# Optimization experiments

Measured on AMD Instinct MI355X. Metric: run time of the kernel, lower is better.

Reference implementation:

```python
import jax, jax.numpy as jnp
import numpy as np
import math

THETA = 10000.0

def _rope(x, pos):
    # x: [B, H, S, Dh], pos: [S]
    d = x.shape[-1]
    inv_freq = 1.0 / (THETA ** (jnp.arange(0, d, 2, dtype=jnp.float32) / d))  # [Dh/2]
    ang = pos.astype(jnp.float32)[:, None] * inv_freq[None, :]                # [S, Dh/2]
    cos, sin = jnp.cos(ang), jnp.sin(ang)
    x1, x2 = x[..., 0::2], x[..., 1::2]
    r1 = x1 * cos - x2 * sin
    r2 = x1 * sin + x2 * cos
    return jnp.stack([r1, r2], axis=-1).reshape(x.shape)

def setup_inputs() -> dict:
    key = jax.random.key(0)
    ks = jax.random.split(key, 5)
    B, S, D = 2, 1024, 2048
    Dkv = 512
    scale = 1.0 / math.sqrt(D)
    return {
        "X": jax.random.normal(ks[0], (B, S, D), dtype=jnp.float32),
        "token_positions": jnp.arange(S, dtype=jnp.int32),
        "q_w": jax.random.normal(ks[1], (D, D), dtype=jnp.float32) * scale,
        "k_w": jax.random.normal(ks[2], (Dkv, D), dtype=jnp.float32) * scale,
        "v_w": jax.random.normal(ks[3], (Dkv, D), dtype=jnp.float32) * scale,
        "o_w": jax.random.normal(ks[4], (D, D), dtype=jnp.float32) * scale,
    }

def reference(X, token_positions, q_w, k_w, v_w, o_w):
    B, S, D = X.shape
    H, Hkv = 32, 8
    Dh = D // H
    G = H // Hkv  # query heads per KV head

    Q = (X @ q_w.T).reshape(B, S, H, Dh).transpose(0, 2, 1, 3)      # [B,H,S,Dh]
    K = (X @ k_w.T).reshape(B, S, Hkv, Dh).transpose(0, 2, 1, 3)    # [B,Hkv,S,Dh]
    V = (X @ v_w.T).reshape(B, S, Hkv, Dh).transpose(0, 2, 1, 3)    # [B,Hkv,S,Dh]

    Q = _rope(Q, token_positions)
    K = _rope(K, token_positions)

    # group query heads: [B, Hkv, G, S, Dh]
    Qg = Q.reshape(B, Hkv, G, S, Dh)
    scores = jnp.einsum('bkgqd,bkld->bkgql', Qg, K) / math.sqrt(Dh)  # [B,Hkv,G,S,S]
    causal = jnp.tril(jnp.ones((S, S), dtype=bool))
    scores = jnp.where(causal, scores, -jnp.inf)
    probs = jax.nn.softmax(scores, axis=-1)
    attn = jnp.einsum('bkgql,bkld->bkgqd', probs, V)                 # [B,Hkv,G,S,Dh]

    attn = attn.reshape(B, H, S, Dh).transpose(0, 2, 1, 3).reshape(B, S, D)
    return attn @ o_w.T
```

## Files before the change

kernel.cpp:

```cpp
#include <hip/hip_runtime.h>

typedef _Float16 f16;
typedef _Float16 half8 __attribute__((ext_vector_type(8), may_alias));
typedef _Float16 half4 __attribute__((ext_vector_type(4), may_alias));
typedef float f32x4 __attribute__((ext_vector_type(4), may_alias));

#define ROPE_KF -0.41524101186092027f

__device__ __forceinline__ void gload_lds16(const f16* g, f16* lds) {
  __builtin_amdgcn_global_load_lds(
      (const __attribute__((address_space(1))) void*)g,
      (__attribute__((address_space(3))) void*)lds, 16, 0, 0);
}

template <int N>
__device__ __forceinline__ void waitcnt_vm() {
  if constexpr (N == 0) asm volatile("s_waitcnt vmcnt(0)" ::: "memory");
  else if constexpr (N == 3) asm volatile("s_waitcnt vmcnt(3)" ::: "memory");
  else if constexpr (N == 4) asm volatile("s_waitcnt vmcnt(4)" ::: "memory");
}

__device__ __forceinline__ half8 rope8(half8 v, float posf, int i0, float scale) {
  half8 r;
#pragma unroll
  for (int p = 0; p < 4; ++p) {
    const float ang = posf * exp2f(ROPE_KF * (float)(i0 + p));
    float s, c;
    sincosf(ang, &s, &c);
    const float x1 = (float)v[2 * p], x2 = (float)v[2 * p + 1];
    r[2 * p]     = (f16)((x1 * c - x2 * s) * scale);
    r[2 * p + 1] = (f16)((x1 * s + x2 * c) * scale);
  }
  return r;
}

__global__ __launch_bounds__(256) void cvt_all(const float* __restrict__ s0, f16* __restrict__ d0, int n0,
                                               const float* __restrict__ s1, f16* __restrict__ d1, int n1,
                                               const float* __restrict__ s2, f16* __restrict__ d2, int n2,
                                               const float* __restrict__ s3, f16* __restrict__ d3, int n3,
                                               const float* __restrict__ s4, f16* __restrict__ d4, int n4) {
  const int step = gridDim.x * blockDim.x * 4;
  const int base = (blockIdx.x * blockDim.x + threadIdx.x) * 4;
  auto go = [&](const float* s, f16* d, int n) {
    for (int i = base; i < n; i += step) {
      float4 v = *(const float4*)(s + i);
      half4 h;
      h[0] = (f16)v.x; h[1] = (f16)v.y; h[2] = (f16)v.z; h[3] = (f16)v.w;
      *(half4*)(d + i) = h;
    }
  };
  go(s0, d0, n0); go(s1, d1, n1); go(s2, d2, n2); go(s3, d3, n3); go(s4, d4, n4);
}

template <int OUT_F32, int BM>
__global__ __launch_bounds__(256, 2) void gemm_bt(const f16* __restrict__ A,
                                                  const f16* __restrict__ B,
                                                  void* __restrict__ Cv,
                                                  int M, int N, int K) {
  constexpr int NJ = (BM == 128) ? 4 : 2;
  constexpr int ACH = BM / 64;
  constexpr int LPS = ACH + 2;

  __shared__ alignas(16) f16 As[2][BM][32];
  __shared__ alignas(16) f16 Bs[2][128][32];
  const int tid = threadIdx.x;
  const int w = tid >> 6, l = tid & 63;
  const int m0 = blockIdx.y * BM, n0 = blockIdx.x << 7;
  const int fr = l & 15;
  const int fkz = (((l >> 4) ^ ((fr >> 1) & 3)) << 3);
  const int wr = (BM == 128) ? ((w >> 1) << 6) : 0;
  const int wc = (BM == 128) ? ((w & 1) << 6) : (w << 5);
  const int srow = l >> 2;
  const int scol = (((l & 3) ^ ((l >> 3) & 3)) << 3);

  const f16* ga = A + (size_t)(m0 + srow) * K + scol;
  const f16* gb = B + (size_t)(n0 + srow) * K + scol;

  auto stage = [&](int buf, int t) {
    const int k0 = t << 5;
#pragma unroll
    for (int c = 0; c < ACH; ++c) {
      const int rb = (w * ACH + c) << 4;
      gload_lds16(ga + (size_t)rb * K + k0, &As[buf][rb][0]);
    }
#pragma unroll
    for (int c = 0; c < 2; ++c) {
      const int rb = (w * 2 + c) << 4;
      gload_lds16(gb + (size_t)rb * K + k0, &Bs[buf][rb][0]);
    }
  };

  f32x4 acc[4][NJ] = {};

  const int nk = K >> 5;
  stage(0, 0);
  stage(1, 1);
  for (int t = 0; t < nk; ++t) {
    const int buf = t & 1;
    if (t + 1 < nk) waitcnt_vm<LPS>();
    else waitcnt_vm<0>();
    __builtin_amdgcn_s_barrier();
    __builtin_amdgcn_sched_barrier(0);
    half8 af[4], bf[NJ];
#pragma unroll
    for (int i = 0; i < 4; ++i) af[i] = *(const half8*)&As[buf][wr + i * 16 + fr][fkz];
#pragma unroll
    for (int j = 0; j < NJ; ++j) bf[j] = *(const half8*)&Bs[buf][wc + j * 16 + fr][fkz];
#pragma unroll
    for (int i = 0; i < 4; ++i)
#pragma unroll
      for (int j = 0; j < NJ; ++j)
        acc[i][j] = __builtin_amdgcn_mfma_f32_16x16x32_f16(af[i], bf[j], acc[i][j], 0, 0, 0);
    __builtin_amdgcn_sched_barrier(0);
    __builtin_amdgcn_s_barrier();
    if (t + 2 < nk) stage(buf, t + 2);
  }

  const int orow = (l >> 4) << 2;
#pragma unroll
  for (int i = 0; i < 4; ++i) {
#pragma unroll
    for (int j = 0; j < NJ; ++j) {
      const int col = n0 + wc + j * 16 + fr;
#pragma unroll
      for (int r = 0; r < 4; ++r) {
        const size_t idx = (size_t)(m0 + wr + i * 16 + orow + r) * N + col;
        if (OUT_F32) ((float*)Cv)[idx] = acc[i][j][r];
        else ((f16*)Cv)[idx] = (f16)acc[i][j][r];
      }
    }
  }
}

__global__ __launch_bounds__(256) void repack_kv(const f16* __restrict__ QKV,
                                                 const int* __restrict__ pos,
                                                 f16* __restrict__ Kp,
                                                 f16* __restrict__ Vt) {
  const int kt = blockIdx.x, kvh = blockIdx.y, b = blockIdx.z;
  const int tid = threadIdx.x;
  __shared__ f16 vs[64][72];
  const size_t tile = ((size_t)((b * 8 + kvh) * 16 + kt)) * 4096;
  const f16* kbase = QKV + 2048 + kvh * 64;
  const f16* vbase = QKV + 2560 + kvh * 64;
#pragma unroll
  for (int p = 0; p < 2; ++p) {
    const int c = tid + p * 256;
    const int row = c >> 3, slot = c & 7;
    const size_t grow = (size_t)(b * 1024 + kt * 64 + row) * 3072;
    half8 kk = *(const half8*)(kbase + grow + slot * 8);
    kk = rope8(kk, (float)pos[kt * 64 + row], slot << 2, 1.0f);
    *(half8*)(Kp + tile + row * 64 + ((slot ^ (row & 7)) << 3)) = kk;
    *(half8*)&vs[row][slot * 8] = *(const half8*)(vbase + grow + slot * 8);
  }
  __syncthreads();
#pragma unroll
  for (int p = 0; p < 2; ++p) {
    const int c = tid + p * 256;
    const int d = c >> 3, oct = c & 7;
    half8 vv;
#pragma unroll
    for (int m = 0; m < 8; ++m) vv[m] = vs[oct * 8 + m][d];
    *(half8*)(Vt + tile + d * 64 + ((oct ^ (d & 7)) << 3)) = vv;
  }
}

__global__ __launch_bounds__(256) void attn_fwd(const f16* __restrict__ QKV,
                                                const f16* __restrict__ Kp,
                                                const f16* __restrict__ Vt,
                                                const int* __restrict__ pos,
                                                f16* __restrict__ O) {
  const int flat = blockIdx.x + (blockIdx.y << 3) + (blockIdx.z << 8);
  const int rmid = ((flat & 7) << 6) + (flat >> 3);
  const int pr = rmid & 7, h = (rmid >> 3) & 31, b = rmid >> 8;
  const int kvh = h >> 2;
  const int tid = threadIdx.x, w = tid >> 6, l = tid & 63;
  const int fr = l & 15, g = l >> 4;
  const int orow = g << 2;
  const int qtA = pr, qtB = 15 - pr;

  __shared__ alignas(16) char KsB[2][8192];
  __shared__ alignas(16) char VtB[2][8192];
  __shared__ alignas(16) f16 Ps[4][16][72];

  auto KS = [&](int buf, int row, int slot) -> f16* {
    return (f16*)(KsB[buf] + row * 128 + ((slot ^ (row & 7)) << 4));
  };
  auto VT = [&](int buf, int d, int oct) -> f16* {
    return (f16*)(VtB[buf] + d * 128 + ((oct ^ (d & 7)) << 4));
  };

  const int sA = qtA * 64 + w * 16 + fr, sB = qtB * 64 + w * 16 + fr;
  const float pA = (float)pos[sA], pB = (float)pos[sB];
  const size_t qoff = (size_t)(b * 1024 + w * 16 + fr) * 3072 + h * 64 + (g << 3);
  const f16* qA = QKV + qoff + (size_t)qtA * 64 * 3072;
  const f16* qB = QKV + qoff + (size_t)qtB * 64 * 3072;
  const half8 aA0 = rope8(*(const half8*)qA, pA, g << 2, 0.125f);
  const half8 aA1 = rope8(*(const half8*)(qA + 32), pA, 16 + (g << 2), 0.125f);
  const half8 aB0 = rope8(*(const half8*)qB, pB, g << 2, 0.125f);
  const half8 aB1 = rope8(*(const half8*)(qB + 32), pB, 16 + (g << 2), 0.125f);

  float rmA[4], rlA[4], rmB[4], rlB[4];
  f32x4 oA[4] = {}, oB[4] = {};
#pragma unroll
  for (int r = 0; r < 4; ++r) { rmA[r] = rmB[r] = -3.0e38f; rlA[r] = rlB[r] = 0.f; }

  const size_t tbase = ((size_t)((b * 8 + kvh) * 16)) * 4096;
  const f16* kp0 = Kp + tbase + w * 1024 + (l << 3);
  const f16* vp0 = Vt + tbase + w * 1024 + (l << 3);
  auto stage = [&](int buf, int kt) {
    const f16* kp = kp0 + (size_t)kt * 4096;
    const f16* vp = vp0 + (size_t)kt * 4096;
    f16* kl = (f16*)(KsB[buf] + w * 2048);
    f16* vl = (f16*)(VtB[buf] + w * 2048);
    gload_lds16(kp, kl);
    gload_lds16(kp + 512, kl + 512);
    gload_lds16(vp, vl);
    gload_lds16(vp + 512, vl + 512);
  };

  auto compute = [&](int buf, const half8& a0, const half8& a1, float* rm, float* rl,
                     f32x4* o, int qt, int kt) {
    f32x4 s4[4] = {};
#pragma unroll
    for (int j = 0; j < 4; ++j) {
      const half8 bk0 = *(const half8*)KS(buf, j * 16 + fr, g);
      const half8 bk1 = *(const half8*)KS(buf, j * 16 + fr, 4 + g);
      s4[j] = __builtin_amdgcn_mfma_f32_16x16x32_f16(a0, bk0, s4[j], 0, 0, 0);
      s4[j] = __builtin_amdgcn_mfma_f32_16x16x32_f16(a1, bk1, s4[j], 0, 0, 0);
    }
    if (kt == qt) {
      const int qrow0 = qt * 64 + w * 16 + orow;
#pragma unroll
      for (int j = 0; j < 4; ++j) {
        const int col = kt * 64 + j * 16 + fr;
#pragma unroll
        for (int r = 0; r < 4; ++r)
          if (col > qrow0 + r) s4[j][r] = -1.0e30f;
      }
    }
#pragma unroll
    for (int r = 0; r < 4; ++r) {
      float mx = fmaxf(fmaxf(s4[0][r], s4[1][r]), fmaxf(s4[2][r], s4[3][r]));
#pragma unroll
      for (int off = 8; off >= 1; off >>= 1) mx = fmaxf(mx, __shfl_xor(mx, off));
      const float mn = fmaxf(rm[r], mx);
      const float sf = __expf(rm[r] - mn);
      rl[r] *= sf;
      o[0][r] *= sf; o[1][r] *= sf; o[2][r] *= sf; o[3][r] *= sf;
      rm[r] = mn;
    }
    float ps[4] = {0.f, 0.f, 0.f, 0.f};
#pragma unroll
    for (int j = 0; j < 4; ++j)
#pragma unroll
      for (int r = 0; r < 4; ++r) {
        const float p = __expf(s4[j][r] - rm[r]);
        ps[r] += p;
        Ps[w][orow + r][j * 16 + fr] = (f16)p;
      }
#pragma unroll
    for (int r = 0; r < 4; ++r) {
      float t = ps[r];
#pragma unroll
      for (int off = 8; off >= 1; off >>= 1) t += __shfl_xor(t, off);
      rl[r] += t;
    }
#pragma unroll
    for (int kv2 = 0; kv2 < 2; ++kv2) {
      const half8 ap = *(const half8*)&Ps[w][fr][kv2 * 32 + (g << 3)];
#pragma unroll
      for (int j = 0; j < 4; ++j) {
        const half8 bv = *(const half8*)VT(buf, j * 16 + fr, kv2 * 4 + g);
        o[j] = __builtin_amdgcn_mfma_f32_16x16x32_f16(ap, bv, o[j], 0, 0, 0);
      }
    }
  };

  stage(0, 0);
  stage(1, 1);
  for (int kt = 0; kt <= qtB; ++kt) {
    const int buf = kt & 1;
    if (kt < qtB) waitcnt_vm<4>();
    else waitcnt_vm<0>();
    __builtin_amdgcn_s_barrier();
    __builtin_amdgcn_sched_barrier(0);
    if (kt <= qtA) compute(buf, aA0, aA1, rmA, rlA, oA, qtA, kt);
    compute(buf, aB0, aB1, rmB, rlB, oB, qtB, kt);
    __builtin_amdgcn_sched_barrier(0);
    __builtin_amdgcn_s_barrier();
    if (kt + 2 <= qtB) stage(buf, kt + 2);
  }

#pragma unroll
  for (int j = 0; j < 4; ++j)
#pragma unroll
    for (int r = 0; r < 4; ++r) {
      const int rowA = qtA * 64 + w * 16 + orow + r;
      const int rowB = qtB * 64 + w * 16 + orow + r;
      const int col = h * 64 + j * 16 + fr;
      O[(size_t)(b * 1024 + rowA) * 2048 + col] = (f16)(oA[j][r] / rlA[r]);
      O[(size_t)(b * 1024 + rowB) * 2048 + col] = (f16)(oB[j][r] / rlB[r]);
    }
}

extern "C" void kernel_launch(void* const* d_in, const int* in_sizes, int n_in,
                              void* d_out, int out_size, void* d_ws, size_t ws_size,
                              hipStream_t stream) {
  const float* X = (const float*)d_in[0];
  const int* tokpos = (const int*)d_in[1];
  const float* qw = (const float*)d_in[2];
  const float* kw = (const float*)d_in[3];
  const float* vw = (const float*)d_in[4];
  const float* ow = (const float*)d_in[5];

  constexpr int B = 2, S = 1024, D = 2048, DKV = 512, H = 32;
  constexpr int M = B * S;
  constexpr int NQKV = D + 2 * DKV;

  char* ws = (char*)d_ws;
  f16* Xh   = (f16*)(ws);
  f16* QKVW = (f16*)(ws + (8u << 20));
  f16* owh  = (f16*)(ws + (20u << 20));
  f16* QKVc = (f16*)(ws + (28u << 20));
  f16* Ah   = (f16*)(ws + (40u << 20));
  f16* Kp   = (f16*)(ws);
  f16* Vt   = (f16*)(ws + (2u << 20));

  cvt_all<<<2048, 256, 0, stream>>>(X, Xh, M * D,
                                    qw, QKVW, D * D,
                                    kw, QKVW + (size_t)D * D, DKV * D,
                                    vw, QKVW + (size_t)(D + DKV) * D, DKV * D,
                                    ow, owh, D * D);

  gemm_bt<0, 128><<<dim3(NQKV / 128, M / 128), 256, 0, stream>>>(Xh, QKVW, QKVc, M, NQKV, D);

  repack_kv<<<dim3(16, 8, 2), 256, 0, stream>>>(QKVc, tokpos, Kp, Vt);

  attn_fwd<<<dim3(8, H, B), 256, 0, stream>>>(QKVc, Kp, Vt, tokpos, Ah);

  gemm_bt<1, 64><<<dim3(D / 128, M / 64), 256, 0, stream>>>(Ah, owh, d_out, M, D, D);
}
```

Measured before the change: 137.5 us.

## Deepen GEMM pipeline to four LDS stages with register-prefetched fragments

The GEMM kernel moves from a two-stage to a four-stage LDS ring buffer and keeps three tiles in flight. It double-buffers the MFMA operand fragments in registers, so the next tile's LDS reads overlap the current tile's MFMAs. The trailing barrier per k-step is dropped, leaving one barrier per step. In exchange it uses twice the LDS and more VGPRs, which could reduce occupancy at two blocks per CU.

Measured after the change: 142.7 us. 3.8% more time.

```diff
diff --git a/kernel.cpp b/kernel.cpp
--- a/kernel.cpp
+++ b/kernel.cpp
@@ -14,10 +14,12 @@
 }
 
 template <int N>
-__device__ __forceinline__ void waitcnt_vm() {
+__device__ __forceinline__ void vm_wait() {
   if constexpr (N == 0) asm volatile("s_waitcnt vmcnt(0)" ::: "memory");
   else if constexpr (N == 3) asm volatile("s_waitcnt vmcnt(3)" ::: "memory");
   else if constexpr (N == 4) asm volatile("s_waitcnt vmcnt(4)" ::: "memory");
+  else if constexpr (N == 6) asm volatile("s_waitcnt vmcnt(6)" ::: "memory");
+  else if constexpr (N == 8) asm volatile("s_waitcnt vmcnt(8)" ::: "memory");
 }
 
 __device__ __forceinline__ half8 rope8(half8 v, float posf, int i0, float scale) {
@@ -61,8 +63,8 @@
   constexpr int ACH = BM / 64;
   constexpr int LPS = ACH + 2;
 
-  __shared__ alignas(16) f16 As[2][BM][32];
-  __shared__ alignas(16) f16 Bs[2][128][32];
+  __shared__ alignas(16) f16 As[4][BM][32];
+  __shared__ alignas(16) f16 Bs[4][128][32];
   const int tid = threadIdx.x;
   const int w = tid >> 6, l = tid & 63;
   const int m0 = blockIdx.y * BM, n0 = blockIdx.x << 7;
@@ -76,8 +78,8 @@
   const f16* ga = A + (size_t)(m0 + srow) * K + scol;
   const f16* gb = B + (size_t)(n0 + srow) * K + scol;
 
-  auto stage = [&](int buf, int t) {
-    const int k0 = t << 5;
+  auto stage = [&](int t) {
+    const int buf = t & 3, k0 = t << 5;
 #pragma unroll
     for (int c = 0; c < ACH; ++c) {
       const int rb = (w * ACH + c) << 4;
@@ -90,30 +92,48 @@
     }
   };
 
+  half8 afA[4], bfA[NJ], afB[4], bfB[NJ];
+  auto readfrags = [&](int t, half8* af, half8* bf) {
+    const int buf = t & 3;
+#pragma unroll
+    for (int i = 0; i < 4; ++i) af[i] = *(const half8*)&As[buf][wr + i * 16 + fr][fkz];
+#pragma unroll
+    for (int j = 0; j < NJ; ++j) bf[j] = *(const half8*)&Bs[buf][wc + j * 16 + fr][fkz];
+  };
+
   f32x4 acc[4][NJ] = {};
+  auto mm = [&](half8* af, half8* bf) {
+#pragma unroll
+    for (int i = 0; i < 4; ++i)
+#pragma unroll
+      for (int j = 0; j < NJ; ++j)
+        acc[i][j] = __builtin_amdgcn_mfma_f32_16x16x32_f16(af[i], bf[j], acc[i][j], 0, 0, 0);
+  };
 
   const int nk = K >> 5;
-  stage(0, 0);
-  stage(1, 1);
-  for (int t = 0; t < nk; ++t) {
-    const int buf = t & 1;
-    if (t + 1 < nk) waitcnt_vm<LPS>();
-    else waitcnt_vm<0>();
+  stage(0); stage(1); stage(2);
+  vm_wait<2 * LPS>();
+  __builtin_amdgcn_s_barrier();
+  __builtin_amdgcn_sched_barrier(0);
+  readfrags(0, afA, bfA);
+
+  for (int t = 0; t < nk; t += 2) {
+    if (t + 2 < nk) vm_wait<LPS>(); else vm_wait<0>();
     __builtin_amdgcn_s_barrier();
     __builtin_amdgcn_sched_barrier(0);
-    half8 af[4], bf[NJ];
-#pragma unroll
-    for (int i = 0; i < 4; ++i) af[i] = *(const half8*)&As[buf][wr + i * 16 + fr][fkz];
-#pragma unroll
-    for (int j = 0; j < NJ; ++j) bf[j] = *(const half8*)&Bs[buf][wc + j * 16 + fr][fkz];
-#pragma unroll
-    for (int i = 0; i < 4; ++i)
-#pragma unroll
-      for (int j = 0; j < NJ; ++j)
-        acc[i][j] = __builtin_amdgcn_mfma_f32_16x16x32_f16(af[i], bf[j], acc[i][j], 0, 0, 0);
+    if (t + 3 < nk) stage(t + 3);
+    if (t + 1 < nk) readfrags(t + 1, afB, bfB);
+    mm(afA, bfA);
     __builtin_amdgcn_sched_barrier(0);
-    __builtin_amdgcn_s_barrier();
-    if (t + 2 < nk) stage(buf, t + 2);
+    if (t + 1 < nk) {
+      if (t + 3 < nk) vm_wait<LPS>(); else vm_wait<0>();
+      __builtin_amdgcn_s_barrier();
+      __builtin_amdgcn_sched_barrier(0);
+      if (t + 4 < nk) stage(t + 4);
+      if (t + 2 < nk) readfrags(t + 2, afA, bfA);
+      mm(afB, bfB);
+      __builtin_amdgcn_sched_barrier(0);
+    }
   }
 
   const int orow = (l >> 4) << 2;
@@ -280,8 +300,8 @@
   stage(1, 1);
   for (int kt = 0; kt <= qtB; ++kt) {
     const int buf = kt & 1;
-    if (kt < qtB) waitcnt_vm<4>();
-    else waitcnt_vm<0>();
+    if (kt < qtB) vm_wait<4>();
+    else vm_wait<0>();
     __builtin_amdgcn_s_barrier();
     __builtin_amdgcn_sched_barrier(0);
     if (kt <= qtA) compute(buf, aA0, aA1, rmA, rlA, oA, qtA, kt);
```

## Rewrite GEMM as single-wave 128x64 tiles with 4-stage barrier-free pipeline

Applied to the files above, without the earlier changes.

Replaces the 256-thread, 4-wave GEMM with a 64-thread, single-wavefront kernel. Each wave computes a 128x64 output tile with an 8x4 MFMA accumulator and uses a 4-deep LDS ring buffer, prefetching two stages ahead and waiting only on vmcnt. Because one wave owns the whole tile, the workgroup barriers go away and more tiles can be resident per CU. The cost is much higher register pressure per wave (128 accumulator floats) and less parallelism per block, which may hurt latency hiding. Both the QKV and output projections now use this kernel.

After: 170.4 us. 23.9% more time.

```diff
diff --git a/kernel.cpp b/kernel.cpp
--- a/kernel.cpp
+++ b/kernel.cpp
@@ -14,10 +14,11 @@
 }
 
 template <int N>
-__device__ __forceinline__ void waitcnt_vm() {
+__device__ __forceinline__ void vm_wait() {
   if constexpr (N == 0) asm volatile("s_waitcnt vmcnt(0)" ::: "memory");
-  else if constexpr (N == 3) asm volatile("s_waitcnt vmcnt(3)" ::: "memory");
   else if constexpr (N == 4) asm volatile("s_waitcnt vmcnt(4)" ::: "memory");
+  else if constexpr (N == 12) asm volatile("s_waitcnt vmcnt(12)" ::: "memory");
+  else if constexpr (N == 24) asm volatile("s_waitcnt vmcnt(24)" ::: "memory");
 }
 
 __device__ __forceinline__ half8 rope8(half8 v, float posf, int i0, float scale) {
@@ -52,79 +53,70 @@
   go(s0, d0, n0); go(s1, d1, n1); go(s2, d2, n2); go(s3, d3, n3); go(s4, d4, n4);
 }
 
-template <int OUT_F32, int BM>
-__global__ __launch_bounds__(256, 2) void gemm_bt(const f16* __restrict__ A,
-                                                  const f16* __restrict__ B,
-                                                  void* __restrict__ Cv,
-                                                  int M, int N, int K) {
-  constexpr int NJ = (BM == 128) ? 4 : 2;
-  constexpr int ACH = BM / 64;
-  constexpr int LPS = ACH + 2;
-
-  __shared__ alignas(16) f16 As[2][BM][32];
-  __shared__ alignas(16) f16 Bs[2][128][32];
-  const int tid = threadIdx.x;
-  const int w = tid >> 6, l = tid & 63;
-  const int m0 = blockIdx.y * BM, n0 = blockIdx.x << 7;
+template <int OUT_F32>
+__global__ __launch_bounds__(64) void gemm_bt(const f16* __restrict__ A,
+                                              const f16* __restrict__ B,
+                                              void* __restrict__ Cv,
+                                              int M, int N, int K) {
+  __shared__ alignas(16) f16 As[4][128][32];
+  __shared__ alignas(16) f16 Bs[4][64][32];
+  const int l = threadIdx.x;
+  const int m0 = blockIdx.y << 7, n0 = blockIdx.x << 6;
   const int fr = l & 15;
   const int fkz = (((l >> 4) ^ ((fr >> 1) & 3)) << 3);
-  const int wr = (BM == 128) ? ((w >> 1) << 6) : 0;
-  const int wc = (BM == 128) ? ((w & 1) << 6) : (w << 5);
   const int srow = l >> 2;
   const int scol = (((l & 3) ^ ((l >> 3) & 3)) << 3);
 
   const f16* ga = A + (size_t)(m0 + srow) * K + scol;
   const f16* gb = B + (size_t)(n0 + srow) * K + scol;
 
-  auto stage = [&](int buf, int t) {
-    const int k0 = t << 5;
-#pragma unroll
-    for (int c = 0; c < ACH; ++c) {
-      const int rb = (w * ACH + c) << 4;
-      gload_lds16(ga + (size_t)rb * K + k0, &As[buf][rb][0]);
-    }
-#pragma unroll
-    for (int c = 0; c < 2; ++c) {
-      const int rb = (w * 2 + c) << 4;
-      gload_lds16(gb + (size_t)rb * K + k0, &Bs[buf][rb][0]);
-    }
-  };
-
-  f32x4 acc[4][NJ] = {};
+  auto stage = [&](int t) {
+    const int buf = t & 3, k0 = t << 5;
+#pragma unroll
+    for (int c = 0; c < 8; ++c)
+      gload_lds16(ga + (size_t)(c << 4) * K + k0, &As[buf][c << 4][0]);
+#pragma unroll
+    for (int c = 0; c < 4; ++c)
+      gload_lds16(gb + (size_t)(c << 4) * K + k0, &Bs[buf][c << 4][0]);
+  };
+
+  f32x4 acc[8][4] = {};
 
   const int nk = K >> 5;
-  stage(0, 0);
-  stage(1, 1);
+  stage(0);
+  stage(1);
   for (int t = 0; t < nk; ++t) {
-    const int buf = t & 1;
-    if (t + 1 < nk) waitcnt_vm<LPS>();
-    else waitcnt_vm<0>();
-    __builtin_amdgcn_s_barrier();
+    if (t + 2 < nk) {
+      stage(t + 2);
+      vm_wait<24>();
+    } else if (t + 1 < nk) {
+      vm_wait<12>();
+    } else {
+      vm_wait<0>();
+    }
     __builtin_amdgcn_sched_barrier(0);
-    half8 af[4], bf[NJ];
-#pragma unroll
-    for (int i = 0; i < 4; ++i) af[i] = *(const half8*)&As[buf][wr + i * 16 + fr][fkz];
-#pragma unroll
-    for (int j = 0; j < NJ; ++j) bf[j] = *(const half8*)&Bs[buf][wc + j * 16 + fr][fkz];
-#pragma unroll
-    for (int i = 0; i < 4; ++i)
-#pragma unroll
-      for (int j = 0; j < NJ; ++j)
+    const int buf = t & 3;
+    half8 af[8], bf[4];
+#pragma unroll
+    for (int j = 0; j < 4; ++j) bf[j] = *(const half8*)&Bs[buf][j * 16 + fr][fkz];
+#pragma unroll
+    for (int i = 0; i < 8; ++i) af[i] = *(const half8*)&As[buf][i * 16 + fr][fkz];
+#pragma unroll
+    for (int i = 0; i < 8; ++i)
+#pragma unroll
+      for (int j = 0; j < 4; ++j)
         acc[i][j] = __builtin_amdgcn_mfma_f32_16x16x32_f16(af[i], bf[j], acc[i][j], 0, 0, 0);
-    __builtin_amdgcn_sched_barrier(0);
-    __builtin_amdgcn_s_barrier();
-    if (t + 2 < nk) stage(buf, t + 2);
   }
 
   const int orow = (l >> 4) << 2;
 #pragma unroll
-  for (int i = 0; i < 4; ++i) {
-#pragma unroll
-    for (int j = 0; j < NJ; ++j) {
-      const int col = n0 + wc + j * 16 + fr;
+  for (int i = 0; i < 8; ++i) {
+#pragma unroll
+    for (int j = 0; j < 4; ++j) {
+      const int col = n0 + j * 16 + fr;
 #pragma unroll
       for (int r = 0; r < 4; ++r) {
-        const size_t idx = (size_t)(m0 + wr + i * 16 + orow + r) * N + col;
+        const size_t idx = (size_t)(m0 + i * 16 + orow + r) * N + col;
         if (OUT_F32) ((float*)Cv)[idx] = acc[i][j][r];
         else ((f16*)Cv)[idx] = (f16)acc[i][j][r];
       }
@@ -280,8 +272,8 @@
   stage(1, 1);
   for (int kt = 0; kt <= qtB; ++kt) {
     const int buf = kt & 1;
-    if (kt < qtB) waitcnt_vm<4>();
-    else waitcnt_vm<0>();
+    if (kt < qtB) vm_wait<4>();
+    else vm_wait<0>();
     __builtin_amdgcn_s_barrier();
     __builtin_amdgcn_sched_barrier(0);
     if (kt <= qtA) compute(buf, aA0, aA1, rmA, rlA, oA, qtA, kt);
@@ -332,11 +324,11 @@
                                     vw, QKVW + (size_t)(D + DKV) * D, DKV * D,
                                     ow, owh, D * D);
 
-  gemm_bt<0, 128><<<dim3(NQKV / 128, M / 128), 256, 0, stream>>>(Xh, QKVW, QKVc, M, NQKV, D);
+  gemm_bt<0><<<dim3(NQKV / 64, M / 128), 64, 0, stream>>>(Xh, QKVW, QKVc, M, NQKV, D);
 
   repack_kv<<<dim3(16, 8, 2), 256, 0, stream>>>(QKVc, tokpos, Kp, Vt);
 
   attn_fwd<<<dim3(8, H, B), 256, 0, stream>>>(QKVc, Kp, Vt, tokpos, Ah);
 
-  gemm_bt<1, 64><<<dim3(D / 128, M / 64), 256, 0, stream>>>(Ah, owh, d_out, M, D, D);
-}
+  gemm_bt<1><<<dim3(D / 64, M / 128), 64, 0, stream>>>(Ah, owh, d_out, M, D, D);
+}
```

## Split-K the QKV projection GEMM and fold the partial sums into consumers

Applied to the files above, without the earlier changes.

The QKV GEMM is launched with two K-splits along gridDim.z. Each split writes its own fp16 partial result buffer (QKVc0 and QKVc1), and repack_kv and attn_fwd add the two partials when they load Q, K and V. The QKV grid is only 24x16 = 384 blocks, so this doubles the parallelism to better fill the many CUs. The cost is extra partial-buffer writes and reads, and the partials are rounded to fp16 before they are summed, which loses some precision. Ah is moved in the workspace to make room for the second buffer.

Result: faster. 132.0 us (median of 5 runs) (-4.0%).

```diff
diff --git a/kernel.cpp b/kernel.cpp
--- a/kernel.cpp
+++ b/kernel.cpp
@@ -14,20 +14,22 @@
 }
 
 template <int N>
-__device__ __forceinline__ void waitcnt_vm() {
+__device__ __forceinline__ void vm_wait() {
   if constexpr (N == 0) asm volatile("s_waitcnt vmcnt(0)" ::: "memory");
   else if constexpr (N == 3) asm volatile("s_waitcnt vmcnt(3)" ::: "memory");
   else if constexpr (N == 4) asm volatile("s_waitcnt vmcnt(4)" ::: "memory");
 }
 
-__device__ __forceinline__ half8 rope8(half8 v, float posf, int i0, float scale) {
+__device__ __forceinline__ half8 rope8s(half8 va, half8 vb, float posf, int i0,
+                                        float scale) {
   half8 r;
 #pragma unroll
   for (int p = 0; p < 4; ++p) {
     const float ang = posf * exp2f(ROPE_KF * (float)(i0 + p));
     float s, c;
     sincosf(ang, &s, &c);
-    const float x1 = (float)v[2 * p], x2 = (float)v[2 * p + 1];
+    const float x1 = (float)va[2 * p] + (float)vb[2 * p];
+    const float x2 = (float)va[2 * p + 1] + (float)vb[2 * p + 1];
     r[2 * p]     = (f16)((x1 * c - x2 * s) * scale);
     r[2 * p + 1] = (f16)((x1 * s + x2 * c) * scale);
   }
@@ -66,6 +68,8 @@
   const int tid = threadIdx.x;
   const int w = tid >> 6, l = tid & 63;
   const int m0 = blockIdx.y * BM, n0 = blockIdx.x << 7;
+  const int klen = K / gridDim.z;
+  const int koff = blockIdx.z * klen;
   const int fr = l & 15;
   const int fkz = (((l >> 4) ^ ((fr >> 1) & 3)) << 3);
   const int wr = (BM == 128) ? ((w >> 1) << 6) : 0;
@@ -73,8 +77,8 @@
   const int srow = l >> 2;
   const int scol = (((l & 3) ^ ((l >> 3) & 3)) << 3);
 
-  const f16* ga = A + (size_t)(m0 + srow) * K + scol;
-  const f16* gb = B + (size_t)(n0 + srow) * K + scol;
+  const f16* ga = A + (size_t)(m0 + srow) * K + koff + scol;
+  const f16* gb = B + (size_t)(n0 + srow) * K + koff + scol;
 
   auto stage = [&](int buf, int t) {
     const int k0 = t << 5;
@@ -92,13 +96,13 @@
 
   f32x4 acc[4][NJ] = {};
 
-  const int nk = K >> 5;
   stage(0, 0);
   stage(1, 1);
+  const int nk = klen >> 5;
   for (int t = 0; t < nk; ++t) {
     const int buf = t & 1;
-    if (t + 1 < nk) waitcnt_vm<LPS>();
-    else waitcnt_vm<0>();
+    if (t + 1 < nk) vm_wait<LPS>();
+    else vm_wait<0>();
     __builtin_amdgcn_s_barrier();
     __builtin_amdgcn_sched_barrier(0);
     half8 af[4], bf[NJ];
@@ -116,6 +120,7 @@
     if (t + 2 < nk) stage(buf, t + 2);
   }
 
+  const size_t zoff = (size_t)blockIdx.z * M * (size_t)N;
   const int orow = (l >> 4) << 2;
 #pragma unroll
   for (int i = 0; i < 4; ++i) {
@@ -124,7 +129,7 @@
       const int col = n0 + wc + j * 16 + fr;
 #pragma unroll
       for (int r = 0; r < 4; ++r) {
-        const size_t idx = (size_t)(m0 + wr + i * 16 + orow + r) * N + col;
+        const size_t idx = zoff + (size_t)(m0 + wr + i * 16 + orow + r) * N + col;
         if (OUT_F32) ((float*)Cv)[idx] = acc[i][j][r];
         else ((f16*)Cv)[idx] = (f16)acc[i][j][r];
       }
@@ -132,7 +137,8 @@
   }
 }
 
-__global__ __launch_bounds__(256) void repack_kv(const f16* __restrict__ QKV,
+__global__ __launch_bounds__(256) void repack_kv(const f16* __restrict__ QKV0,
+                                                 const f16* __restrict__ QKV1,
                                                  const int* __restrict__ pos,
                                                  f16* __restrict__ Kp,
                                                  f16* __restrict__ Vt) {
@@ -140,17 +146,22 @@
   const int tid = threadIdx.x;
   __shared__ f16 vs[64][72];
   const size_t tile = ((size_t)((b * 8 + kvh) * 16 + kt)) * 4096;
-  const f16* kbase = QKV + 2048 + kvh * 64;
-  const f16* vbase = QKV + 2560 + kvh * 64;
+  const size_t kcol = 2048 + kvh * 64, vcol = 2560 + kvh * 64;
 #pragma unroll
   for (int p = 0; p < 2; ++p) {
     const int c = tid + p * 256;
     const int row = c >> 3, slot = c & 7;
-    const size_t grow = (size_t)(b * 1024 + kt * 64 + row) * 3072;
-    half8 kk = *(const half8*)(kbase + grow + slot * 8);
-    kk = rope8(kk, (float)pos[kt * 64 + row], slot << 2, 1.0f);
+    const size_t grow = (size_t)(b * 1024 + kt * 64 + row) * 3072 + slot * 8;
+    const half8 k0 = *(const half8*)(QKV0 + grow + kcol);
+    const half8 k1 = *(const half8*)(QKV1 + grow + kcol);
+    const half8 kk = rope8s(k0, k1, (float)pos[kt * 64 + row], slot << 2, 1.0f);
     *(half8*)(Kp + tile + row * 64 + ((slot ^ (row & 7)) << 3)) = kk;
-    *(half8*)&vs[row][slot * 8] = *(const half8*)(vbase + grow + slot * 8);
+    const half8 v0 = *(const half8*)(QKV0 + grow + vcol);
+    const half8 v1 = *(const half8*)(QKV1 + grow + vcol);
+    half8 vv;
+#pragma unroll
+    for (int ii = 0; ii < 8; ++ii) vv[ii] = (f16)((float)v0[ii] + (float)v1[ii]);
+    *(half8*)&vs[row][slot * 8] = vv;
   }
   __syncthreads();
 #pragma unroll
@@ -164,7 +175,8 @@
   }
 }
 
-__global__ __launch_bounds__(256) void attn_fwd(const f16* __restrict__ QKV,
+__global__ __launch_bounds__(256) void attn_fwd(const f16* __restrict__ QKV0,
+                                                const f16* __restrict__ QKV1,
                                                 const f16* __restrict__ Kp,
                                                 const f16* __restrict__ Vt,
                                                 const int* __restrict__ pos,
@@ -192,12 +204,16 @@
   const int sA = qtA * 64 + w * 16 + fr, sB = qtB * 64 + w * 16 + fr;
   const float pA = (float)pos[sA], pB = (float)pos[sB];
   const size_t qoff = (size_t)(b * 1024 + w * 16 + fr) * 3072 + h * 64 + (g << 3);
-  const f16* qA = QKV + qoff + (size_t)qtA * 64 * 3072;
-  const f16* qB = QKV + qoff + (size_t)qtB * 64 * 3072;
-  const half8 aA0 = rope8(*(const half8*)qA, pA, g << 2, 0.125f);
-  const half8 aA1 = rope8(*(const half8*)(qA + 32), pA, 16 + (g << 2), 0.125f);
-  const half8 aB0 = rope8(*(const half8*)qB, pB, g << 2, 0.125f);
-  const half8 aB1 = rope8(*(const half8*)(qB + 32), pB, 16 + (g << 2), 0.125f);
+  const size_t qoA = qoff + (size_t)qtA * 64 * 3072;
+  const size_t qoB = qoff + (size_t)qtB * 64 * 3072;
+  const half8 aA0 = rope8s(*(const half8*)(QKV0 + qoA), *(const half8*)(QKV1 + qoA),
+                           pA, g << 2, 0.125f);
+  const half8 aA1 = rope8s(*(const half8*)(QKV0 + qoA + 32), *(const half8*)(QKV1 + qoA + 32),
+                           pA, 16 + (g << 2), 0.125f);
+  const half8 aB0 = rope8s(*(const half8*)(QKV0 + qoB), *(const half8*)(QKV1 + qoB),
+                           pB, g << 2, 0.125f);
+  const half8 aB1 = rope8s(*(const half8*)(QKV0 + qoB + 32), *(const half8*)(QKV1 + qoB + 32),
+                           pB, 16 + (g << 2), 0.125f);
 
   float rmA[4], rlA[4], rmB[4], rlB[4];
   f32x4 oA[4] = {}, oB[4] = {};
@@ -280,8 +296,8 @@
   stage(1, 1);
   for (int kt = 0; kt <= qtB; ++kt) {
     const int buf = kt & 1;
-    if (kt < qtB) waitcnt_vm<4>();
-    else waitcnt_vm<0>();
+    if (kt < qtB) vm_wait<4>();
+    else vm_wait<0>();
     __builtin_amdgcn_s_barrier();
     __builtin_amdgcn_sched_barrier(0);
     if (kt <= qtA) compute(buf, aA0, aA1, rmA, rlA, oA, qtA, kt);
@@ -318,13 +334,14 @@
   constexpr int NQKV = D + 2 * DKV;
 
   char* ws = (char*)d_ws;
-  f16* Xh   = (f16*)(ws);
-  f16* QKVW = (f16*)(ws + (8u << 20));
-  f16* owh  = (f16*)(ws + (20u << 20));
-  f16* QKVc = (f16*)(ws + (28u << 20));
-  f16* Ah   = (f16*)(ws + (40u << 20));
-  f16* Kp   = (f16*)(ws);
-  f16* Vt   = (f16*)(ws + (2u << 20));
+  f16* Xh    = (f16*)(ws);
+  f16* QKVW  = (f16*)(ws + (8u << 20));
+  f16* owh   = (f16*)(ws + (20u << 20));
+  f16* QKVc0 = (f16*)(ws + (28u << 20));
+  f16* QKVc1 = (f16*)(ws + (40u << 20));
+  f16* Kp    = (f16*)(ws);
+  f16* Vt    = (f16*)(ws + (2u << 20));
+  f16* Ah    = (f16*)(ws + (4u << 20));
 
   cvt_all<<<2048, 256, 0, stream>>>(X, Xh, M * D,
                                     qw, QKVW, D * D,
@@ -332,11 +349,12 @@
                                     vw, QKVW + (size_t)(D + DKV) * D, DKV * D,
                                     ow, owh, D * D);
 
-  gemm_bt<0, 128><<<dim3(NQKV / 128, M / 128), 256, 0, stream>>>(Xh, QKVW, QKVc, M, NQKV, D);
-
-  repack_kv<<<dim3(16, 8, 2), 256, 0, stream>>>(QKVc, tokpos, Kp, Vt);
-
-  attn_fwd<<<dim3(8, H, B), 256, 0, stream>>>(QKVc, Kp, Vt, tokpos, Ah);
-
-  gemm_bt<1, 64><<<dim3(D / 128, M / 64), 256, 0, stream>>>(Ah, owh, d_out, M, D, D);
-}
+  gemm_bt<0, 128><<<dim3(NQKV / 128, M / 128, 2), 256, 0, stream>>>(Xh, QKVW, QKVc0,
+                                                                    M, NQKV, D);
+
+  repack_kv<<<dim3(16, 8, 2), 256, 0, stream>>>(QKVc0, QKVc1, tokpos, Kp, Vt);
+
+  attn_fwd<<<dim3(8, H, B), 256, 0, stream>>>(QKVc0, QKVc1, Kp, Vt, tokpos, Ah);
+
+  gemm_bt<1, 64><<<dim3(D / 128, M / 64, 1), 256, 0, stream>>>(Ah, owh, d_out, M, D, D);
+}
```
